# Kernel tuning notes

Hardware: AMD Instinct MI355X
Metric: run time of the kernel (lower is better)

The kernel has to match this reference:

```python
import jax, jax.numpy as jnp
import numpy as np

N = 1_000_000
D = 256
B = 4096


def setup_inputs() -> dict:
    key = jax.random.key(0)
    ks = jax.random.split(key, 8)
    s = 1.0 / np.sqrt(D)
    x = jax.random.normal(ks[0], (N, D), dtype=jnp.float32)
    batch = jnp.sort(jax.random.randint(ks[1], (N,), 0, B, dtype=jnp.int64))
    W1 = jax.random.normal(ks[2], (D, D), dtype=jnp.float32) * s
    b1 = jax.random.normal(ks[3], (D,), dtype=jnp.float32) * s
    w2 = jax.random.normal(ks[4], (D,), dtype=jnp.float32) * s
    b2 = jax.random.normal(ks[5], (), dtype=jnp.float32) * s
    Wp = jax.random.normal(ks[6], (D, D), dtype=jnp.float32) * s
    bp = jax.random.normal(ks[7], (D,), dtype=jnp.float32) * s
    return {"x": x, "batch": batch, "W1": W1, "b1": b1, "w2": w2,
            "b2": b2, "Wp": Wp, "bp": bp}


def reference(x, batch, W1, b1, w2, b2, Wp, bp):
    # score MLP: Linear -> tanh -> Linear(->1), squeezed to (N,)
    s = jnp.tanh(x @ W1 + b1) @ w2 + b2  # (N,)
    # numerically stable segment softmax over graphs
    g_max = jax.ops.segment_max(s, batch, num_segments=B)          # (B,)
    e = jnp.exp(s - g_max[batch])                                   # (N,)
    denom = jax.ops.segment_sum(e, batch, num_segments=B)          # (B,)
    alpha = e / denom[batch]                                        # (N,)
    # weighted scatter-add pooling: (B, D)
    pooled = jax.ops.segment_sum(alpha[:, None] * x, batch, num_segments=B)
    return pooled @ Wp + bp                                         # (B, D_out)
```

## Files before the change

kernel.cpp:

```cpp
#include <hip/hip_runtime.h>


typedef __bf16 bf16_t;
typedef __attribute__((ext_vector_type(8))) __bf16 bf16x8;
typedef __attribute__((ext_vector_type(4))) float f32x4;

constexpr int D = 256;

__global__ void prep_wfrag_kernel(const float* __restrict__ W1,
                                  bf16_t* __restrict__ wfrag) {
    int tid = blockIdx.x * blockDim.x + threadIdx.x;
    if (tid >= 16 * 8 * 64) return;
    int lane = tid & 63;
    int kk   = (tid >> 6) & 7;
    int j    = tid >> 9;
    int quad = lane >> 4, col = lane & 15;
    const float* src = W1 + (size_t)(kk * 32 + quad * 8) * D + j * 16 + col;
    bf16_t* dst = wfrag + (size_t)tid * 8;
#pragma unroll
    for (int t = 0; t < 8; ++t) dst[t] = (bf16_t)src[(size_t)t * D];
}

__global__ __launch_bounds__(256, 2) void scores_kernel(
    const float* __restrict__ x, const bf16_t* __restrict__ wfrag,
    const float* __restrict__ b1, const float* __restrict__ w2,
    float* __restrict__ s, int N) {
    const int lane = threadIdx.x & 63;
    const int wave = threadIdx.x >> 6;
    const int quad = lane >> 4;
    const int col  = lane & 15;
    const long base = (long)blockIdx.x * 256 + wave * 64;

    bf16x8 A[4][8];
#pragma unroll
    for (int st = 0; st < 4; ++st) {
        long row = base + st * 16 + col;
        if (row >= N) row = N - 1;
        const float* xp = x + row * (long)D + quad * 8;
#pragma unroll
        for (int kk = 0; kk < 8; ++kk) {
            float4 u0 = *(const float4*)(xp + kk * 32);
            float4 u1 = *(const float4*)(xp + kk * 32 + 4);
            bf16x8 a;
            a[0] = (bf16_t)u0.x; a[1] = (bf16_t)u0.y;
            a[2] = (bf16_t)u0.z; a[3] = (bf16_t)u0.w;
            a[4] = (bf16_t)u1.x; a[5] = (bf16_t)u1.y;
            a[6] = (bf16_t)u1.z; a[7] = (bf16_t)u1.w;
            A[st][kk] = a;
        }
    }

    float spart[4][4];
#pragma unroll
    for (int st = 0; st < 4; ++st)
#pragma unroll
        for (int r = 0; r < 4; ++r) spart[st][r] = 0.f;

    for (int j = 0; j < 16; ++j) {
        f32x4 C[4];
#pragma unroll
        for (int st = 0; st < 4; ++st)
#pragma unroll
            for (int r = 0; r < 4; ++r) C[st][r] = 0.f;
#pragma unroll
        for (int kk = 0; kk < 8; ++kk) {
            bf16x8 Bf = *(const bf16x8*)(wfrag +
                        (size_t)((j * 8 + kk) * 64 + lane) * 8);
#pragma unroll
            for (int st = 0; st < 4; ++st)
                C[st] = __builtin_amdgcn_mfma_f32_16x16x32_bf16(
                    A[st][kk], Bf, C[st], 0, 0, 0);
        }
        int n = j * 16 + col;
        float w2n = w2[n];
        float b1n = b1[n];
#pragma unroll
        for (int st = 0; st < 4; ++st)
#pragma unroll
            for (int r = 0; r < 4; ++r) {
                float h = C[st][r] + b1n;
                float e = __expf(2.f * h);
                spart[st][r] += (1.f - 2.f / (e + 1.f)) * w2n;
            }
    }
#pragma unroll
    for (int o = 1; o < 16; o <<= 1)
#pragma unroll
        for (int st = 0; st < 4; ++st)
#pragma unroll
            for (int r = 0; r < 4; ++r)
                spart[st][r] += __shfl_xor(spart[st][r], o, 64);
    if (col == 0) {
#pragma unroll
        for (int st = 0; st < 4; ++st)
#pragma unroll
            for (int r = 0; r < 4; ++r) {
                long row = base + st * 16 + quad * 4 + r;
                if (row < N) s[row] = spart[st][r];
            }
    }
}

__global__ void seg_offsets_kernel(const int* __restrict__ batch,
                                   int* __restrict__ off, int N, int B) {
    int b = blockIdx.x * blockDim.x + threadIdx.x;
    if (b > B) return;
    int lo = 0, hi = N;
    while (lo < hi) {
        int mid = (lo + hi) >> 1;
        if (batch[mid] < b) lo = mid + 1; else hi = mid;
    }
    off[b] = lo;
}

constexpr int CHUNK = 512;
__global__ __launch_bounds__(256) void pool_kernel(
    const float* __restrict__ x, const float* __restrict__ s,
    const int* __restrict__ off, float* __restrict__ pooled) {
    const int b = blockIdx.x;
    const int t = threadIdx.x;
    const int beg = off[b], end = off[b + 1];
    __shared__ float red[256];
    __shared__ float alpha[CHUNK];

    float m = -INFINITY;
    for (int i = beg + t; i < end; i += 256) m = fmaxf(m, s[i]);
    red[t] = m;
    __syncthreads();
    for (int k = 128; k > 0; k >>= 1) {
        if (t < k) red[t] = fmaxf(red[t], red[t + k]);
        __syncthreads();
    }
    m = red[0];
    __syncthreads();

    float dsum = 0.f;
    for (int i = beg + t; i < end; i += 256) dsum += __expf(s[i] - m);
    red[t] = dsum;
    __syncthreads();
    for (int k = 128; k > 0; k >>= 1) {
        if (t < k) red[t] += red[t + k];
        __syncthreads();
    }
    float dinv = red[0] > 0.f ? 1.f / red[0] : 0.f;

    float acc = 0.f;
    for (int c = beg; c < end; c += CHUNK) {
        int len = min(CHUNK, end - c);
        __syncthreads();
        for (int i = t; i < len; i += 256)
            alpha[i] = __expf(s[c + i] - m) * dinv;
        __syncthreads();
        for (int i = 0; i < len; ++i)
            acc += alpha[i] * x[(size_t)(c + i) * D + t];
    }
    pooled[(size_t)b * D + t] = acc;
}

__global__ __launch_bounds__(256) void out_gemm_kernel(
    const float* __restrict__ pooled, const float* __restrict__ Wp,
    const float* __restrict__ bp, float* __restrict__ out) {
    constexpr int GR = 8;
    int rb = blockIdx.x * GR;
    int j = threadIdx.x;
    __shared__ float P[D * GR];
    for (int i = threadIdx.x; i < GR * D; i += 256) {
        int r = i >> 8, k = i & 255;
        P[k * GR + r] = pooled[(size_t)(rb + r) * D + k];
    }
    __syncthreads();
    float acc[GR];
#pragma unroll
    for (int r = 0; r < GR; ++r) acc[r] = 0.f;
    for (int k = 0; k < D; ++k) {
        float w = Wp[(size_t)k * D + j];
        const float4* p4 = (const float4*)(&P[k * GR]);
        float4 a = p4[0], c = p4[1];
        acc[0] += a.x * w; acc[1] += a.y * w; acc[2] += a.z * w; acc[3] += a.w * w;
        acc[4] += c.x * w; acc[5] += c.y * w; acc[6] += c.z * w; acc[7] += c.w * w;
    }
    float bj = bp[j];
#pragma unroll
    for (int r = 0; r < GR; ++r) out[(size_t)(rb + r) * D + j] = acc[r] + bj;
}

extern "C" void kernel_launch(void* const* d_in, const int* in_sizes, int n_in,
                              void* d_out, int out_size, void* d_ws, size_t ws_size,
                              hipStream_t stream) {
    const float* x     = (const float*)d_in[0];
    const int*   batch = (const int*)d_in[1];
    const float* W1    = (const float*)d_in[2];
    const float* b1    = (const float*)d_in[3];
    const float* w2    = (const float*)d_in[4];
    const float* Wp    = (const float*)d_in[6];
    const float* bp    = (const float*)d_in[7];
    float* out = (float*)d_out;
    const int N = in_sizes[1];
    const int B = out_size / D;

    char* w = (char*)d_ws;
    bf16_t* wfrag = (bf16_t*)w;
    size_t off_s = 131072;
    float* s = (float*)(w + off_s);
    size_t off_off = off_s + (size_t)4 * N;
    int* off = (int*)(w + off_off);
    size_t off_pooled = (off_off + 4 * (size_t)(B + 1) + 15) & ~(size_t)15;
    float* pooled = (float*)(w + off_pooled);

    hipLaunchKernelGGL(prep_wfrag_kernel, dim3(32), dim3(256), 0, stream,
                       W1, wfrag);
    int nb = (N + 255) / 256;
    hipLaunchKernelGGL(scores_kernel, dim3(nb), dim3(256), 0, stream,
                       x, wfrag, b1, w2, s, N);
    hipLaunchKernelGGL(seg_offsets_kernel, dim3((B + 1 + 255) / 256), dim3(256),
                       0, stream, batch, off, N, B);
    hipLaunchKernelGGL(pool_kernel, dim3(B), dim3(256), 0, stream,
                       x, s, off, pooled);
    hipLaunchKernelGGL(out_gemm_kernel, dim3(B / 8), dim3(256), 0, stream,
                       pooled, Wp, bp, out);
}
```

Before: 1.674 ms.

## Fuse score MLP with softmax pooling through per-segment atomics

Merges the score computation and the segment softmax pooling into one kernel. Each block computes exp(score) for its 256 rows and re-reads those rows of x while they are likely still cached. It accumulates per-segment weighted sums and denominators and flushes them with atomicAdd when the segment id changes. Normalisation by the denominator moves into the output GEMM, which removes the separate offsets kernel, the score buffer and the second full pass over x. Dropping the max subtraction risks overflow for large scores, and the atomics make the float summation order nondeterministic.

```diff
diff --git a/kernel.cpp b/kernel.cpp
--- a/kernel.cpp
+++ b/kernel.cpp
@@ -7,29 +7,49 @@
 
 constexpr int D = 256;
 
-__global__ void prep_wfrag_kernel(const float* __restrict__ W1,
-                                  bf16_t* __restrict__ wfrag) {
+__global__ void prep_kernel(const float* __restrict__ W1,
+                            bf16_t* __restrict__ wfrag,
+                            float* __restrict__ pooled_raw,
+                            float* __restrict__ denom, int B) {
     int tid = blockIdx.x * blockDim.x + threadIdx.x;
-    if (tid >= 16 * 8 * 64) return;
-    int lane = tid & 63;
-    int kk   = (tid >> 6) & 7;
-    int j    = tid >> 9;
-    int quad = lane >> 4, col = lane & 15;
-    const float* src = W1 + (size_t)(kk * 32 + quad * 8) * D + j * 16 + col;
-    bf16_t* dst = wfrag + (size_t)tid * 8;
-#pragma unroll
-    for (int t = 0; t < 8; ++t) dst[t] = (bf16_t)src[(size_t)t * D];
-}
-
-__global__ __launch_bounds__(256, 2) void scores_kernel(
-    const float* __restrict__ x, const bf16_t* __restrict__ wfrag,
-    const float* __restrict__ b1, const float* __restrict__ w2,
-    float* __restrict__ s, int N) {
+    if (tid < B * D / 4) ((float4*)pooled_raw)[tid] = make_float4(0.f, 0.f, 0.f, 0.f);
+    if (tid < B / 4) ((float4*)denom)[tid] = make_float4(0.f, 0.f, 0.f, 0.f);
+    if (tid < 16 * 8 * 64) {
+        int lane = tid & 63;
+        int kk   = (tid >> 6) & 7;
+        int j    = tid >> 9;
+        int quad = lane >> 4, col = lane & 15;
+        const float* src = W1 + (size_t)(kk * 32 + quad * 8) * D + j * 16 + col;
+        bf16_t* dst = wfrag + (size_t)tid * 8;
+#pragma unroll
+        for (int t = 0; t < 8; ++t) dst[t] = (bf16_t)src[(size_t)t * D];
+    }
+}
+
+__global__ __launch_bounds__(256, 2) void fused_kernel(
+    const float* __restrict__ x, const int* __restrict__ batch,
+    const bf16_t* __restrict__ wfrag, const float* __restrict__ b1,
+    const float* __restrict__ w2, float* __restrict__ pooled_raw,
+    float* __restrict__ denom, int N) {
     const int lane = threadIdx.x & 63;
     const int wave = threadIdx.x >> 6;
     const int quad = lane >> 4;
     const int col  = lane & 15;
-    const long base = (long)blockIdx.x * 256 + wave * 64;
+    const int bb   = blockIdx.x * 256;
+    const long base = (long)bb + wave * 64;
+
+    __shared__ float e_lds[256];
+    __shared__ int   batch_lds[257];
+
+    {
+        int t = threadIdx.x;
+        long r = bb + t; if (r >= N) r = N - 1;
+        batch_lds[t] = batch[r];
+        if (t == 0) {
+            long r2 = bb + 255; if (r2 >= N) r2 = N - 1;
+            batch_lds[256] = batch[r2];
+        }
+    }
 
     bf16x8 A[4][8];
 #pragma unroll
@@ -79,8 +99,8 @@
 #pragma unroll
             for (int r = 0; r < 4; ++r) {
                 float h = C[st][r] + b1n;
-                float e = __expf(2.f * h);
-                spart[st][r] += (1.f - 2.f / (e + 1.f)) * w2n;
+                float ex = __expf(2.f * h);
+                spart[st][r] += (1.f - 2.f / (ex + 1.f)) * w2n;
             }
     }
 #pragma unroll
@@ -96,77 +116,49 @@
 #pragma unroll
             for (int r = 0; r < 4; ++r) {
                 long row = base + st * 16 + quad * 4 + r;
-                if (row < N) s[row] = spart[st][r];
+                e_lds[row - bb] = (row < N) ? __expf(spart[st][r]) : 0.f;
             }
     }
-}
-
-__global__ void seg_offsets_kernel(const int* __restrict__ batch,
-                                   int* __restrict__ off, int N, int B) {
-    int b = blockIdx.x * blockDim.x + threadIdx.x;
-    if (b > B) return;
-    int lo = 0, hi = N;
-    while (lo < hi) {
-        int mid = (lo + hi) >> 1;
-        if (batch[mid] < b) lo = mid + 1; else hi = mid;
-    }
-    off[b] = lo;
-}
-
-constexpr int CHUNK = 512;
-__global__ __launch_bounds__(256) void pool_kernel(
-    const float* __restrict__ x, const float* __restrict__ s,
-    const int* __restrict__ off, float* __restrict__ pooled) {
-    const int b = blockIdx.x;
-    const int t = threadIdx.x;
-    const int beg = off[b], end = off[b + 1];
-    __shared__ float red[256];
-    __shared__ float alpha[CHUNK];
-
-    float m = -INFINITY;
-    for (int i = beg + t; i < end; i += 256) m = fmaxf(m, s[i]);
-    red[t] = m;
     __syncthreads();
-    for (int k = 128; k > 0; k >>= 1) {
-        if (t < k) red[t] = fmaxf(red[t], red[t + k]);
-        __syncthreads();
-    }
-    m = red[0];
-    __syncthreads();
-
-    float dsum = 0.f;
-    for (int i = beg + t; i < end; i += 256) dsum += __expf(s[i] - m);
-    red[t] = dsum;
-    __syncthreads();
-    for (int k = 128; k > 0; k >>= 1) {
-        if (t < k) red[t] += red[t + k];
-        __syncthreads();
-    }
-    float dinv = red[0] > 0.f ? 1.f / red[0] : 0.f;
-
-    float acc = 0.f;
-    for (int c = beg; c < end; c += CHUNK) {
-        int len = min(CHUNK, end - c);
-        __syncthreads();
-        for (int i = t; i < len; i += 256)
-            alpha[i] = __expf(s[c + i] - m) * dinv;
-        __syncthreads();
-        for (int i = 0; i < len; ++i)
-            acc += alpha[i] * x[(size_t)(c + i) * D + t];
-    }
-    pooled[(size_t)b * D + t] = acc;
+
+    {
+        const int t = threadIdx.x;
+        float acc = 0.f, acc_e = 0.f;
+#pragma unroll 4
+        for (int i = 0; i < 256; ++i) {
+            long row = bb + i; if (row >= N) row = N - 1;
+            float e  = e_lds[i];
+            float xv = x[row * (long)D + t];
+            acc   += e * xv;
+            acc_e += e;
+            bool flush = (i == 255) || (batch_lds[i + 1] != batch_lds[i]);
+            if (flush) {
+                int seg = batch_lds[i];
+                atomicAdd(&pooled_raw[(size_t)seg * D + t], acc);
+                if (t == 0) atomicAdd(&denom[seg], acc_e);
+                acc = 0.f; acc_e = 0.f;
+            }
+        }
+    }
 }
 
 __global__ __launch_bounds__(256) void out_gemm_kernel(
-    const float* __restrict__ pooled, const float* __restrict__ Wp,
-    const float* __restrict__ bp, float* __restrict__ out) {
+    const float* __restrict__ pooled_raw, const float* __restrict__ denom,
+    const float* __restrict__ Wp, const float* __restrict__ bp,
+    float* __restrict__ out) {
     constexpr int GR = 8;
     int rb = blockIdx.x * GR;
     int j = threadIdx.x;
     __shared__ float P[D * GR];
+    __shared__ float dv[GR];
+    if (j < GR) {
+        float d = denom[rb + j];
+        dv[j] = d > 0.f ? 1.f / d : 0.f;
+    }
+    __syncthreads();
     for (int i = threadIdx.x; i < GR * D; i += 256) {
         int r = i >> 8, k = i & 255;
-        P[k * GR + r] = pooled[(size_t)(rb + r) * D + k];
+        P[k * GR + r] = pooled_raw[(size_t)(rb + r) * D + k] * dv[r];
     }
     __syncthreads();
     float acc[GR];
@@ -200,22 +192,15 @@
 
     char* w = (char*)d_ws;
     bf16_t* wfrag = (bf16_t*)w;
-    size_t off_s = 131072;
-    float* s = (float*)(w + off_s);
-    size_t off_off = off_s + (size_t)4 * N;
-    int* off = (int*)(w + off_off);
-    size_t off_pooled = (off_off + 4 * (size_t)(B + 1) + 15) & ~(size_t)15;
-    float* pooled = (float*)(w + off_pooled);
-
-    hipLaunchKernelGGL(prep_wfrag_kernel, dim3(32), dim3(256), 0, stream,
-                       W1, wfrag);
+    float* pooled_raw = (float*)(w + 131072);
+    float* denom = (float*)(w + 131072 + (size_t)4 * B * D);
+
+    int zthreads = B * D / 4;
+    hipLaunchKernelGGL(prep_kernel, dim3((zthreads + 255) / 256), dim3(256), 0,
+                       stream, W1, wfrag, pooled_raw, denom, B);
     int nb = (N + 255) / 256;
-    hipLaunchKernelGGL(scores_kernel, dim3(nb), dim3(256), 0, stream,
-                       x, wfrag, b1, w2, s, N);
-    hipLaunchKernelGGL(seg_offsets_kernel, dim3((B + 1 + 255) / 256), dim3(256),
-                       0, stream, batch, off, N, B);
-    hipLaunchKernelGGL(pool_kernel, dim3(B), dim3(256), 0, stream,
-                       x, s, off, pooled);
+    hipLaunchKernelGGL(fused_kernel, dim3(nb), dim3(256), 0, stream,
+                       x, batch, wfrag, b1, w2, pooled_raw, denom, N);
     hipLaunchKernelGGL(out_gemm_kernel, dim3(B / 8), dim3(256), 0, stream,
-                       pooled, Wp, bp, out);
-}
+                       pooled_raw, denom, Wp, bp, out);
+}
```

After: 2.102 ms. 25.6% more time.
